# Performance work log

Hardware: AMD Instinct MI355X
Metric: run time of the kernel (lower is better)

The kernel has to match this reference:

```python
import jax, jax.numpy as jnp
import numpy as np

EPS = 1e-6
INPUT_SIZE = 64
NUM_LEAVES = INPUT_SIZE
NUM_LAYERS = NUM_LEAVES - 1
BATCH = 262144
SINKHORN_ITERS = 20


def _clip01(v):
    return jnp.clip(v, EPS, 1.0 - EPS)


def _F_base(x, y, a, w0, w1):
    # Branches of F for a in [0.5, 2] (the non-recursive region), selected branchlessly.
    x = _clip01(x)
    y = _clip01(y)
    lin = w0 * x + w1 * y
    p = jnp.sqrt(3.0 / jnp.maximum(2.0 - a, EPS)) - 1.0
    g = (x ** (2.0 * w0) * y ** (2.0 * w1)) ** p
    rule0 = jnp.where((jnp.abs(x - 1.0) < EPS) & (jnp.abs(y - 1.0) < EPS), 1.0, 0.0)
    return jnp.where(
        jnp.abs(a - 2.0) < EPS, rule0,
        jnp.where(a >= 0.75, g,
                  jnp.where(a > 0.5, (3.0 - 4.0 * a) * lin + (4.0 * a - 2.0) * g, lin)))


def _F(x, y, a, w0, w1):
    # Full generalized_gcd F with the single-level De Morgan reflection for a < 0.5.
    x = _clip01(x)
    y = _clip01(y)
    hi = _F_base(x, y, a, w0, w1)
    a_ref = jnp.clip(1.0 - a, -1.0 + EPS, 2.0 - EPS)
    lo = 1.0 - _F_base(1.0 - x, 1.0 - y, a_ref, w0, w1)
    lin = w0 * x + w1 * y
    return jnp.where(jnp.abs(a - 0.5) < EPS, lin, jnp.where(a < 0.5, lo, hi))


def _sinkhorn(logits, n_iter=SINKHORN_ITERS):
    # Log-space Sinkhorn normalization -> (approximately) doubly-stochastic P.
    l = logits
    for _ in range(n_iter):
        l = l - jax.nn.logsumexp(l, axis=1, keepdims=True)
        l = l - jax.nn.logsumexp(l, axis=0, keepdims=True)
    return jnp.exp(l)


def setup_inputs() -> dict:
    key = jax.random.key(0)
    k1, k2, k3, k4 = jax.random.split(key, 4)
    x = jax.random.uniform(k1, (BATCH, INPUT_SIZE), dtype=jnp.float32)
    logits = jax.random.normal(k2, (INPUT_SIZE, NUM_LEAVES), dtype=jnp.float32)
    weights = jax.random.uniform(k3, (NUM_LAYERS,), dtype=jnp.float32)
    biases = jax.random.uniform(k4, (NUM_LAYERS,), dtype=jnp.float32)
    return {"x": x, "logits": logits, "weights": weights, "biases": biases}


def reference(x, logits, weights, biases):
    P = _sinkhorn(logits)                 # [INPUT_SIZE, NUM_LEAVES], columns sum to 1
    leaves = (x @ P).T                    # [NUM_LEAVES, BATCH]

    def step(carry, inp):
        leaf, w, b = inp
        nres = _F(carry, leaf, b, w, 1.0 - w)
        nres = jnp.where(jnp.isnan(nres), b, nres)  # NaN fallback to bias, as in torch forward
        return nres, None

    # Left-leaning tree: state_0 = leaf_0; state_i = F(state_{i-1}, leaf_i, b, w, 1-w)
    final, _ = jax.lax.scan(step, leaves[0], (leaves[1:], weights, biases))
    return final[:, None]                 # [BATCH, 1]
```

## Files before the change

### kernel.cpp

```cpp
#include <hip/hip_runtime.h>
#include <hip/hip_bf16.h>
#include <math.h>

#define EPS 1e-6f
#define NLAYERS 63
#define SINK_ITERS 20
#define LOG2E 1.4426950408889634f

typedef __attribute__((ext_vector_type(8))) short bf16x8;
typedef __attribute__((ext_vector_type(4))) float f32x4;
typedef __attribute__((ext_vector_type(4))) unsigned int ui32x4;

__device__ __forceinline__ float fast_log2(float v) {
#if __has_builtin(__builtin_amdgcn_logf)
  return __builtin_amdgcn_logf(v);
#else
  return log2f(v);
#endif
}
__device__ __forceinline__ float fast_exp2(float v) {
#if __has_builtin(__builtin_amdgcn_exp2f)
  return __builtin_amdgcn_exp2f(v);
#else
  return exp2f(v);
#endif
}

__device__ __forceinline__ unsigned int f2bf(float f) {
  unsigned int u = __float_as_uint(f);
  return (u + 0x7FFFu + ((u >> 16) & 1u)) >> 16;
}

__device__ __forceinline__ unsigned int cvt_pk_bf16(float lo, float hi) {
  unsigned int r;
  asm("v_cvt_pk_bf16_f32 %0, %1, %2" : "=v"(r) : "v"(lo), "v"(hi));
  return r;
}
__device__ __forceinline__ bf16x8 pack8(float4 a, float4 b) {
  ui32x4 u;
  u[0] = cvt_pk_bf16(a.x, a.y);
  u[1] = cvt_pk_bf16(a.z, a.w);
  u[2] = cvt_pk_bf16(b.x, b.y);
  u[3] = cvt_pk_bf16(b.z, b.w);
  return __builtin_bit_cast(bf16x8, u);
}


template<int HALF>
__device__ __forceinline__ void do_gemm(const bf16x8 (&Bf)[2][4],
                                        const bf16x8 (&Af)[4][2],
                                        float* Lv, int w, int q, int c) {
  #pragma unroll
  for (int rt = 0; rt < 4; ++rt) {
    #pragma unroll
    for (int lt = 0; lt < 2; ++lt) {
      f32x4 acc = {0.f, 0.f, 0.f, 0.f};
      acc = __builtin_amdgcn_mfma_f32_16x16x32_bf16(Bf[0][(HALF << 1) + lt], Af[rt][0], acc, 0, 0, 0);
      acc = __builtin_amdgcn_mfma_f32_16x16x32_bf16(Bf[1][(HALF << 1) + lt], Af[rt][1], acc, 0, 0, 0);
      const int row  = (w << 6) + (rt << 4) + c;
      const int nloc = (lt << 4) + (q << 2);
      *(f32x4*)&Lv[row * 36 + nloc] = acc;
    }
  }
}

template<int L0>
__device__ __forceinline__ void do_chunk(const float* Lrow,
                                         const float* Lcst, float& r) {
  constexpr int loc = L0 & 31;
  f32x4 lf0 = *(const f32x4*)&Lrow[loc];
  f32x4 lf1 = *(const f32x4*)&Lrow[loc + 4];
  float lf[8] = {lf0[0], lf0[1], lf0[2], lf0[3], lf1[0], lf1[1], lf1[2], lf1[3]};

  float ylin[8], ylg[8];
  #pragma unroll
  for (int k = 0; k < 8; ++k) {
    if (L0 + k >= 1) {
      float4 p0 = *(const float4*)&Lcst[(L0 + k - 1) * 8];
      float off = fmaf(-0.5f, p0.x, 0.5f);
      float yy  = fminf(fmaxf(lf[k], EPS), 1.0f - EPS);
      float yr  = fmaf(p0.x, yy, off);
      float ly  = fast_log2(yr);
      ylg[k]  = fmaf(p0.y, ly, p0.z);
      ylin[k] = p0.w * yr;
    }
  }

  #pragma unroll
  for (int k = 0; k < 8; ++k) {
    if (L0 + k >= 1) {
      float4 p1 = *(const float4*)&Lcst[(L0 + k - 1) * 8 + 4];
      float cr = fminf(fmaxf(r, EPS), 1.0f - EPS);
      float xr = fmaf(p1.x, cr, p1.y);
      float lx = fast_log2(xr);
      float g  = fast_exp2(fmaf(p1.z, lx, ylg[k]));
      r = fmaf(p1.w, xr, ylin[k]) + g;
    } else {
      r = lf[0];
    }
  }
}

__global__ __launch_bounds__(256, 4) void fused_kernel(
    const float* __restrict__ x,
    const float* __restrict__ logits,
    const float* __restrict__ weights,
    const float* __restrict__ biases,
    float* __restrict__ out) {
  __shared__ float SMEM[10104];
  float* Lv   = SMEM;
  float* T    = SMEM;
  float* Lcst = SMEM + 9216;
  float* part = SMEM + 9720;
  float* Uv   = SMEM + 9976;
  float* Vv   = SMEM + 10040;

  const int tid = threadIdx.x;
  const int w = tid >> 6, l = tid & 63;
  const int q = l >> 4, c = l & 15;
  const size_t rowbase = (size_t)blockIdx.x << 8;

  bf16x8 Af[4][2];
  {
    const float* rp0 = x + (rowbase + (w << 6) + c) * 64 + (q << 3);
    float4 t0[4], t1[4];
    #define LOADROW(dst, i) do {                                   \
      const float* rp = rp0 + ((i) << 4) * 64;                     \
      (dst)[0] = *(const float4*)(rp);                             \
      (dst)[1] = *(const float4*)(rp + 4);                         \
      (dst)[2] = *(const float4*)(rp + 32);                        \
      (dst)[3] = *(const float4*)(rp + 36);                        \
    } while (0)
    LOADROW(t0, 0);
    LOADROW(t1, 1);
    Af[0][0] = pack8(t0[0], t0[1]); Af[0][1] = pack8(t0[2], t0[3]);
    LOADROW(t0, 2);
    Af[1][0] = pack8(t1[0], t1[1]); Af[1][1] = pack8(t1[2], t1[3]);
    LOADROW(t1, 3);
    Af[2][0] = pack8(t0[0], t0[1]); Af[2][1] = pack8(t0[2], t0[3]);
    Af[3][0] = pack8(t1[0], t1[1]); Af[3][1] = pack8(t1[2], t1[3]);
    #undef LOADROW
  }

  if (tid < NLAYERS) {
    float w0 = weights[tid];
    float w1 = 1.0f - w0;
    float a  = biases[tid];
    float sgn, e0, e1, cw0, cw1, lcg;
    if (fabsf(a - 0.5f) < EPS) {
      sgn = 1.f; e0 = 0.f; e1 = 0.f; cw0 = w0; cw1 = w1; lcg = -1.0e30f;
    } else {
      float ae;
      if (a < 0.5f) { sgn = -1.f; ae = fminf(fmaxf(1.0f - a, -1.0f + EPS), 2.0f - EPS); }
      else          { sgn =  1.f; ae = a; }
      float pp = sqrtf(3.0f / fmaxf(2.0f - ae, EPS)) - 1.0f;
      float cl, cg;
      if (ae >= 0.75f) { cl = 0.0f;            cg = 1.0f; }
      else             { cl = 3.0f - 4.0f*ae;  cg = 4.0f*ae - 2.0f; }
      e0  = 2.0f * w0 * pp;
      e1  = 2.0f * w1 * pp;
      cw0 = cl * w0;
      cw1 = cl * w1;
      lcg = (cg > 0.f) ? log2f(cg) : -1.0e30f;
    }
    float sgnp = 1.f;
    if (tid > 0) {
      float ap = biases[tid - 1];
      sgnp = (fabsf(ap - 0.5f) < EPS) ? 1.f : (ap < 0.5f ? -1.f : 1.f);
    }
    float Sc = sgn * sgnp;
    float Oc = 0.5f - 0.5f * Sc;
    float* Lr = Lcst + tid * 8;
    Lr[0] = sgn; Lr[1] = e1; Lr[2] = lcg; Lr[3] = cw1;
    Lr[4] = Sc;  Lr[5] = Oc; Lr[6] = e0;  Lr[7] = cw0;
  }

  float K_part[16], KT_part[16];
  {
    const float4* lr = (const float4*)(logits + (l << 6) + (w << 4));
    #pragma unroll
    for (int i = 0; i < 4; ++i) {
      float4 t = lr[i];
      K_part[4*i+0] = fast_exp2(t.x * LOG2E);
      K_part[4*i+1] = fast_exp2(t.y * LOG2E);
      K_part[4*i+2] = fast_exp2(t.z * LOG2E);
      K_part[4*i+3] = fast_exp2(t.w * LOG2E);
    }
  }
  #pragma unroll
  for (int i = 0; i < 16; ++i) T[l * 65 + (w << 4) + i] = K_part[i];
  if (tid < 64) Vv[tid] = 1.0f;
  __syncthreads();
  #pragma unroll
  for (int i = 0; i < 16; ++i) KT_part[i] = T[((w << 4) + i) * 65 + l];

  for (int it = 0; it < SINK_ITERS; ++it) {
    float p0 = 0.f, p1 = 0.f, p2 = 0.f, p3 = 0.f;
    #pragma unroll
    for (int i = 0; i < 4; ++i) {
      p0 = fmaf(K_part[4*i+0], Vv[(w << 4) + 4*i+0], p0);
      p1 = fmaf(K_part[4*i+1], Vv[(w << 4) + 4*i+1], p1);
      p2 = fmaf(K_part[4*i+2], Vv[(w << 4) + 4*i+2], p2);
      p3 = fmaf(K_part[4*i+3], Vv[(w << 4) + 4*i+3], p3);
    }
    part[(w << 6) + l] = (p0 + p1) + (p2 + p3);
    __syncthreads();
    if (tid < 64) {
      float s = (part[tid] + part[64 + tid]) + (part[128 + tid] + part[192 + tid]);
      Uv[tid] = 1.0f / s;
    }
    __syncthreads();
    float q0 = 0.f, q1 = 0.f, q2 = 0.f, q3 = 0.f;
    #pragma unroll
    for (int i = 0; i < 4; ++i) {
      q0 = fmaf(KT_part[4*i+0], Uv[(w << 4) + 4*i+0], q0);
      q1 = fmaf(KT_part[4*i+1], Uv[(w << 4) + 4*i+1], q1);
      q2 = fmaf(KT_part[4*i+2], Uv[(w << 4) + 4*i+2], q2);
      q3 = fmaf(KT_part[4*i+3], Uv[(w << 4) + 4*i+3], q3);
    }
    part[(w << 6) + l] = (q0 + q1) + (q2 + q3);
    __syncthreads();
    if (tid < 64) {
      float s = (part[tid] + part[64 + tid]) + (part[128 + tid] + part[192 + tid]);
      Vv[tid] = 1.0f / s;
    }
    __syncthreads();
  }

  {
    const float ul = Uv[l];
    #pragma unroll
    for (int i = 0; i < 16; ++i)
      T[l * 65 + (w << 4) + i] = ul * K_part[i] * Vv[(w << 4) + i];
  }
  __syncthreads();

  bf16x8 Bf[2][4];
  #pragma unroll
  for (int s = 0; s < 2; ++s)
    #pragma unroll
    for (int t = 0; t < 4; ++t) {
      ui32x4 u;
      #pragma unroll
      for (int jj = 0; jj < 4; ++jj) {
        unsigned int lo = f2bf(T[(s*32 + (q << 3) + 2*jj    ) * 65 + t*16 + c]);
        unsigned int hi = f2bf(T[(s*32 + (q << 3) + 2*jj + 1) * 65 + t*16 + c]);
        u[jj] = lo | (hi << 16);
      }
      Bf[s][t] = __builtin_bit_cast(bf16x8, u);
    }
  __syncthreads();

  const float* Lrow = &Lv[tid * 36];
  float r = 0.f;

  do_gemm<0>(Bf, Af, Lv, w, q, c);
  do_chunk<0>(Lrow, Lcst, r);
  do_chunk<8>(Lrow, Lcst, r);
  do_chunk<16>(Lrow, Lcst, r);
  do_chunk<24>(Lrow, Lcst, r);

  do_gemm<1>(Bf, Af, Lv, w, q, c);
  do_chunk<32>(Lrow, Lcst, r);
  do_chunk<40>(Lrow, Lcst, r);
  do_chunk<48>(Lrow, Lcst, r);
  do_chunk<56>(Lrow, Lcst, r);

  const float sgnL = Lcst[62 * 8];
  out[rowbase + tid] = fmaf(sgnL, r, fmaf(-0.5f, sgnL, 0.5f));
}

extern "C" void kernel_launch(void* const* d_in, const int* in_sizes, int n_in,
                              void* d_out, int out_size, void* d_ws, size_t ws_size,
                              hipStream_t stream) {
  const float* x       = (const float*)d_in[0];
  const float* logits  = (const float*)d_in[1];
  const float* weights = (const float*)d_in[2];
  const float* biases  = (const float*)d_in[3];
  float* out = (float*)d_out;

  const int batch = out_size;
  hipLaunchKernelGGL(fused_kernel, dim3(batch / 256), dim3(256), 0, stream,
                     x, logits, weights, biases, out);
}
```

Measured before the change: 119.9 us.

## Split Sinkhorn into a single-block pre-kernel and stream precomputed fragments

Before, every one of the 1024 blocks recomputed the 20-iteration Sinkhorn normalization and the per-layer constants. Now one small kernel computes them once and writes bf16 MFMA B-fragments and the layer constants to workspace. The main scan kernel then loads them from global memory, and its LDS use drops to the Lv buffer only. In exchange it adds a second launch, a serial dependency on a single-block kernel, and global (cached) reads of the layer constants instead of LDS reads.

```diff
diff --git a/kernel.cpp b/kernel.cpp
--- a/kernel.cpp
+++ b/kernel.cpp
@@ -46,6 +46,130 @@
 }
 
 
+__global__ __launch_bounds__(256) void sinkhorn_kernel(
+    const float* __restrict__ logits,
+    const float* __restrict__ weights,
+    const float* __restrict__ biases,
+    unsigned short* __restrict__ Pfrag,
+    float* __restrict__ layers) {
+  __shared__ float T[64 * 65];
+  __shared__ float Uv[64];
+  __shared__ float Vv[64];
+  __shared__ float part[256];
+
+  const int tid = threadIdx.x;
+  const int w = tid >> 6, l = tid & 63;
+  const int q = l >> 4, c = l & 15;
+
+  if (tid < NLAYERS) {
+    float w0 = weights[tid];
+    float w1 = 1.0f - w0;
+    float a  = biases[tid];
+    float sgn, e0, e1, cw0, cw1, lcg;
+    if (fabsf(a - 0.5f) < EPS) {
+      sgn = 1.f; e0 = 0.f; e1 = 0.f; cw0 = w0; cw1 = w1; lcg = -1.0e30f;
+    } else {
+      float ae;
+      if (a < 0.5f) { sgn = -1.f; ae = fminf(fmaxf(1.0f - a, -1.0f + EPS), 2.0f - EPS); }
+      else          { sgn =  1.f; ae = a; }
+      float pp = sqrtf(3.0f / fmaxf(2.0f - ae, EPS)) - 1.0f;
+      float cl, cg;
+      if (ae >= 0.75f) { cl = 0.0f;            cg = 1.0f; }
+      else             { cl = 3.0f - 4.0f*ae;  cg = 4.0f*ae - 2.0f; }
+      e0  = 2.0f * w0 * pp;
+      e1  = 2.0f * w1 * pp;
+      cw0 = cl * w0;
+      cw1 = cl * w1;
+      lcg = (cg > 0.f) ? log2f(cg) : -1.0e30f;
+    }
+    float sgnp = 1.f;
+    if (tid > 0) {
+      float ap = biases[tid - 1];
+      sgnp = (fabsf(ap - 0.5f) < EPS) ? 1.f : (ap < 0.5f ? -1.f : 1.f);
+    }
+    float Sc = sgn * sgnp;
+    float Oc = 0.5f - 0.5f * Sc;
+    float* Lr = layers + tid * 8;
+    Lr[0] = sgn; Lr[1] = e1; Lr[2] = lcg; Lr[3] = cw1;
+    Lr[4] = Sc;  Lr[5] = Oc; Lr[6] = e0;  Lr[7] = cw0;
+  }
+
+  float K_part[16], KT_part[16];
+  {
+    const float4* lr = (const float4*)(logits + (l << 6) + (w << 4));
+    #pragma unroll
+    for (int i = 0; i < 4; ++i) {
+      float4 t = lr[i];
+      K_part[4*i+0] = fast_exp2(t.x * LOG2E);
+      K_part[4*i+1] = fast_exp2(t.y * LOG2E);
+      K_part[4*i+2] = fast_exp2(t.z * LOG2E);
+      K_part[4*i+3] = fast_exp2(t.w * LOG2E);
+    }
+  }
+  #pragma unroll
+  for (int i = 0; i < 16; ++i) T[l * 65 + (w << 4) + i] = K_part[i];
+  if (tid < 64) Vv[tid] = 1.0f;
+  __syncthreads();
+  #pragma unroll
+  for (int i = 0; i < 16; ++i) KT_part[i] = T[((w << 4) + i) * 65 + l];
+
+  for (int it = 0; it < SINK_ITERS; ++it) {
+    float p0 = 0.f, p1 = 0.f, p2 = 0.f, p3 = 0.f;
+    #pragma unroll
+    for (int i = 0; i < 4; ++i) {
+      p0 = fmaf(K_part[4*i+0], Vv[(w << 4) + 4*i+0], p0);
+      p1 = fmaf(K_part[4*i+1], Vv[(w << 4) + 4*i+1], p1);
+      p2 = fmaf(K_part[4*i+2], Vv[(w << 4) + 4*i+2], p2);
+      p3 = fmaf(K_part[4*i+3], Vv[(w << 4) + 4*i+3], p3);
+    }
+    part[(w << 6) + l] = (p0 + p1) + (p2 + p3);
+    __syncthreads();
+    if (tid < 64) {
+      float s = (part[tid] + part[64 + tid]) + (part[128 + tid] + part[192 + tid]);
+      Uv[tid] = 1.0f / s;
+    }
+    __syncthreads();
+    float q0 = 0.f, q1 = 0.f, q2 = 0.f, q3 = 0.f;
+    #pragma unroll
+    for (int i = 0; i < 4; ++i) {
+      q0 = fmaf(KT_part[4*i+0], Uv[(w << 4) + 4*i+0], q0);
+      q1 = fmaf(KT_part[4*i+1], Uv[(w << 4) + 4*i+1], q1);
+      q2 = fmaf(KT_part[4*i+2], Uv[(w << 4) + 4*i+2], q2);
+      q3 = fmaf(KT_part[4*i+3], Uv[(w << 4) + 4*i+3], q3);
+    }
+    part[(w << 6) + l] = (q0 + q1) + (q2 + q3);
+    __syncthreads();
+    if (tid < 64) {
+      float s = (part[tid] + part[64 + tid]) + (part[128 + tid] + part[192 + tid]);
+      Vv[tid] = 1.0f / s;
+    }
+    __syncthreads();
+  }
+
+  {
+    const float ul = Uv[l];
+    #pragma unroll
+    for (int i = 0; i < 16; ++i)
+      T[l * 65 + (w << 4) + i] = ul * K_part[i] * Vv[(w << 4) + i];
+  }
+  __syncthreads();
+
+  #pragma unroll
+  for (int fi = 0; fi < 2; ++fi) {
+    const int f = (w << 1) + fi;
+    const int s = f >> 2, t = f & 3;
+    ui32x4 u;
+    #pragma unroll
+    for (int jj = 0; jj < 4; ++jj) {
+      unsigned int lo = f2bf(T[(s*32 + (q << 3) + 2*jj    ) * 65 + t*16 + c]);
+      unsigned int hi = f2bf(T[(s*32 + (q << 3) + 2*jj + 1) * 65 + t*16 + c]);
+      u[jj] = lo | (hi << 16);
+    }
+    *(ui32x4*)(Pfrag + ((f * 64 + l) << 3)) = u;
+  }
+}
+
+
 template<int HALF>
 __device__ __forceinline__ void do_gemm(const bf16x8 (&Bf)[2][4],
                                         const bf16x8 (&Af)[4][2],
@@ -66,7 +190,7 @@
 
 template<int L0>
 __device__ __forceinline__ void do_chunk(const float* Lrow,
-                                         const float* Lcst, float& r) {
+                                         const float4* Lp4, float& r) {
   constexpr int loc = L0 & 31;
   f32x4 lf0 = *(const f32x4*)&Lrow[loc];
   f32x4 lf1 = *(const f32x4*)&Lrow[loc + 4];
@@ -76,7 +200,7 @@
   #pragma unroll
   for (int k = 0; k < 8; ++k) {
     if (L0 + k >= 1) {
-      float4 p0 = *(const float4*)&Lcst[(L0 + k - 1) * 8];
+      float4 p0 = Lp4[(L0 + k - 1) * 2];
       float off = fmaf(-0.5f, p0.x, 0.5f);
       float yy  = fminf(fmaxf(lf[k], EPS), 1.0f - EPS);
       float yr  = fmaf(p0.x, yy, off);
@@ -89,7 +213,7 @@
   #pragma unroll
   for (int k = 0; k < 8; ++k) {
     if (L0 + k >= 1) {
-      float4 p1 = *(const float4*)&Lcst[(L0 + k - 1) * 8 + 4];
+      float4 p1 = Lp4[(L0 + k - 1) * 2 + 1];
       float cr = fminf(fmaxf(r, EPS), 1.0f - EPS);
       float xr = fmaf(p1.x, cr, p1.y);
       float lx = fast_log2(xr);
@@ -101,24 +225,17 @@
   }
 }
 
-__global__ __launch_bounds__(256, 4) void fused_kernel(
+__global__ __launch_bounds__(256, 4) void scan_kernel(
     const float* __restrict__ x,
-    const float* __restrict__ logits,
-    const float* __restrict__ weights,
-    const float* __restrict__ biases,
+    const unsigned short* __restrict__ Pfrag,
+    const float* __restrict__ layers,
     float* __restrict__ out) {
-  __shared__ float SMEM[10104];
-  float* Lv   = SMEM;
-  float* T    = SMEM;
-  float* Lcst = SMEM + 9216;
-  float* part = SMEM + 9720;
-  float* Uv   = SMEM + 9976;
-  float* Vv   = SMEM + 10040;
-
+  __shared__ float Lv[256 * 36];
   const int tid = threadIdx.x;
   const int w = tid >> 6, l = tid & 63;
   const int q = l >> 4, c = l & 15;
   const size_t rowbase = (size_t)blockIdx.x << 8;
+  const float4* Lp4 = (const float4*)layers;
 
   bf16x8 Af[4][2];
   {
@@ -142,131 +259,29 @@
     #undef LOADROW
   }
 
-  if (tid < NLAYERS) {
-    float w0 = weights[tid];
-    float w1 = 1.0f - w0;
-    float a  = biases[tid];
-    float sgn, e0, e1, cw0, cw1, lcg;
-    if (fabsf(a - 0.5f) < EPS) {
-      sgn = 1.f; e0 = 0.f; e1 = 0.f; cw0 = w0; cw1 = w1; lcg = -1.0e30f;
-    } else {
-      float ae;
-      if (a < 0.5f) { sgn = -1.f; ae = fminf(fmaxf(1.0f - a, -1.0f + EPS), 2.0f - EPS); }
-      else          { sgn =  1.f; ae = a; }
-      float pp = sqrtf(3.0f / fmaxf(2.0f - ae, EPS)) - 1.0f;
-      float cl, cg;
-      if (ae >= 0.75f) { cl = 0.0f;            cg = 1.0f; }
-      else             { cl = 3.0f - 4.0f*ae;  cg = 4.0f*ae - 2.0f; }
-      e0  = 2.0f * w0 * pp;
-      e1  = 2.0f * w1 * pp;
-      cw0 = cl * w0;
-      cw1 = cl * w1;
-      lcg = (cg > 0.f) ? log2f(cg) : -1.0e30f;
-    }
-    float sgnp = 1.f;
-    if (tid > 0) {
-      float ap = biases[tid - 1];
-      sgnp = (fabsf(ap - 0.5f) < EPS) ? 1.f : (ap < 0.5f ? -1.f : 1.f);
-    }
-    float Sc = sgn * sgnp;
-    float Oc = 0.5f - 0.5f * Sc;
-    float* Lr = Lcst + tid * 8;
-    Lr[0] = sgn; Lr[1] = e1; Lr[2] = lcg; Lr[3] = cw1;
-    Lr[4] = Sc;  Lr[5] = Oc; Lr[6] = e0;  Lr[7] = cw0;
-  }
-
-  float K_part[16], KT_part[16];
-  {
-    const float4* lr = (const float4*)(logits + (l << 6) + (w << 4));
-    #pragma unroll
-    for (int i = 0; i < 4; ++i) {
-      float4 t = lr[i];
-      K_part[4*i+0] = fast_exp2(t.x * LOG2E);
-      K_part[4*i+1] = fast_exp2(t.y * LOG2E);
-      K_part[4*i+2] = fast_exp2(t.z * LOG2E);
-      K_part[4*i+3] = fast_exp2(t.w * LOG2E);
-    }
-  }
-  #pragma unroll
-  for (int i = 0; i < 16; ++i) T[l * 65 + (w << 4) + i] = K_part[i];
-  if (tid < 64) Vv[tid] = 1.0f;
-  __syncthreads();
-  #pragma unroll
-  for (int i = 0; i < 16; ++i) KT_part[i] = T[((w << 4) + i) * 65 + l];
-
-  for (int it = 0; it < SINK_ITERS; ++it) {
-    float p0 = 0.f, p1 = 0.f, p2 = 0.f, p3 = 0.f;
-    #pragma unroll
-    for (int i = 0; i < 4; ++i) {
-      p0 = fmaf(K_part[4*i+0], Vv[(w << 4) + 4*i+0], p0);
-      p1 = fmaf(K_part[4*i+1], Vv[(w << 4) + 4*i+1], p1);
-      p2 = fmaf(K_part[4*i+2], Vv[(w << 4) + 4*i+2], p2);
-      p3 = fmaf(K_part[4*i+3], Vv[(w << 4) + 4*i+3], p3);
-    }
-    part[(w << 6) + l] = (p0 + p1) + (p2 + p3);
-    __syncthreads();
-    if (tid < 64) {
-      float s = (part[tid] + part[64 + tid]) + (part[128 + tid] + part[192 + tid]);
-      Uv[tid] = 1.0f / s;
-    }
-    __syncthreads();
-    float q0 = 0.f, q1 = 0.f, q2 = 0.f, q3 = 0.f;
-    #pragma unroll
-    for (int i = 0; i < 4; ++i) {
-      q0 = fmaf(KT_part[4*i+0], Uv[(w << 4) + 4*i+0], q0);
-      q1 = fmaf(KT_part[4*i+1], Uv[(w << 4) + 4*i+1], q1);
-      q2 = fmaf(KT_part[4*i+2], Uv[(w << 4) + 4*i+2], q2);
-      q3 = fmaf(KT_part[4*i+3], Uv[(w << 4) + 4*i+3], q3);
-    }
-    part[(w << 6) + l] = (q0 + q1) + (q2 + q3);
-    __syncthreads();
-    if (tid < 64) {
-      float s = (part[tid] + part[64 + tid]) + (part[128 + tid] + part[192 + tid]);
-      Vv[tid] = 1.0f / s;
-    }
-    __syncthreads();
-  }
-
-  {
-    const float ul = Uv[l];
-    #pragma unroll
-    for (int i = 0; i < 16; ++i)
-      T[l * 65 + (w << 4) + i] = ul * K_part[i] * Vv[(w << 4) + i];
-  }
-  __syncthreads();
-
   bf16x8 Bf[2][4];
   #pragma unroll
   for (int s = 0; s < 2; ++s)
     #pragma unroll
-    for (int t = 0; t < 4; ++t) {
-      ui32x4 u;
-      #pragma unroll
-      for (int jj = 0; jj < 4; ++jj) {
-        unsigned int lo = f2bf(T[(s*32 + (q << 3) + 2*jj    ) * 65 + t*16 + c]);
-        unsigned int hi = f2bf(T[(s*32 + (q << 3) + 2*jj + 1) * 65 + t*16 + c]);
-        u[jj] = lo | (hi << 16);
-      }
-      Bf[s][t] = __builtin_bit_cast(bf16x8, u);
-    }
-  __syncthreads();
+    for (int t = 0; t < 4; ++t)
+      Bf[s][t] = *(const bf16x8*)(Pfrag + (((s*4 + t) * 64 + l) << 3));
 
   const float* Lrow = &Lv[tid * 36];
   float r = 0.f;
 
   do_gemm<0>(Bf, Af, Lv, w, q, c);
-  do_chunk<0>(Lrow, Lcst, r);
-  do_chunk<8>(Lrow, Lcst, r);
-  do_chunk<16>(Lrow, Lcst, r);
-  do_chunk<24>(Lrow, Lcst, r);
+  do_chunk<0>(Lrow, Lp4, r);
+  do_chunk<8>(Lrow, Lp4, r);
+  do_chunk<16>(Lrow, Lp4, r);
+  do_chunk<24>(Lrow, Lp4, r);
 
   do_gemm<1>(Bf, Af, Lv, w, q, c);
-  do_chunk<32>(Lrow, Lcst, r);
-  do_chunk<40>(Lrow, Lcst, r);
-  do_chunk<48>(Lrow, Lcst, r);
-  do_chunk<56>(Lrow, Lcst, r);
-
-  const float sgnL = Lcst[62 * 8];
+  do_chunk<32>(Lrow, Lp4, r);
+  do_chunk<40>(Lrow, Lp4, r);
+  do_chunk<48>(Lrow, Lp4, r);
+  do_chunk<56>(Lrow, Lp4, r);
+
+  const float sgnL = layers[62 * 8];
   out[rowbase + tid] = fmaf(sgnL, r, fmaf(-0.5f, sgnL, 0.5f));
 }
 
@@ -279,7 +294,13 @@
   const float* biases  = (const float*)d_in[3];
   float* out = (float*)d_out;
 
+  unsigned short* Pfrag = (unsigned short*)d_ws;
+  float* layers = (float*)((char*)d_ws + 8 * 64 * 8 * sizeof(unsigned short));
+
   const int batch = out_size;
-  hipLaunchKernelGGL(fused_kernel, dim3(batch / 256), dim3(256), 0, stream,
-                     x, logits, weights, biases, out);
-}
+
+  hipLaunchKernelGGL(sinkhorn_kernel, dim3(1), dim3(256), 0, stream,
+                     logits, weights, biases, Pfrag, layers);
+  hipLaunchKernelGGL(scan_kernel, dim3(batch / 256), dim3(256), 0, stream,
+                     x, Pfrag, layers, out);
+}
```

New measurement: 115.4 us, median of 2. 1.04x faster.
